# Optimization experiments

Hardware: AMD Instinct MI355X
Metric: run time of the kernel (lower is better)

Reference implementation:

```python
import jax, jax.numpy as jnp
import numpy as np

N_HEADS = 8
FACTOR = 5


def setup_inputs() -> dict:
    key = jax.random.key(0)
    ks = jax.random.split(key, 8)
    B, L, D = 2, 4096, 512
    sample_k = min(FACTOR * int(np.ceil(np.log(L))), L)  # 45
    inp = {
        "queries": jax.random.normal(ks[0], (B, L, D), jnp.float32),
        "keys": jax.random.normal(ks[1], (B, L, D), jnp.float32),
        "values": jax.random.normal(ks[2], (B, L, D), jnp.float32),
        "Wq": jax.random.normal(ks[3], (D, D), jnp.float32) * 0.02,
        "bq": jnp.zeros((D,), jnp.float32),
        "Wk": jax.random.normal(ks[4], (D, D), jnp.float32) * 0.02,
        "bk": jnp.zeros((D,), jnp.float32),
        "Wv": jax.random.normal(ks[5], (D, D), jnp.float32) * 0.02,
        "bv": jnp.zeros((D,), jnp.float32),
        "index_sample": jax.random.randint(ks[6], (L, sample_k), 0, L, jnp.int32),
    }
    return inp


def reference(queries, keys, values, Wq, bq, Wk, bk, Wv, bv, index_sample):
    b, l_q, d_model = queries.shape
    _, l_k, _ = keys.shape
    h = N_HEADS
    d = d_model // h
    # projections -> [b, h, l, d]
    q = (queries @ Wq + bq).reshape(b, l_q, h, d).transpose(0, 2, 1, 3)
    k = (keys @ Wk + bk).reshape(b, l_k, h, d).transpose(0, 2, 1, 3)
    v = (values @ Wv + bv).reshape(b, l_k, h, d).transpose(0, 2, 1, 3)
    n_top = min(FACTOR * int(np.ceil(np.log(l_q))), l_q)
    # --- prob_qk: sparse sampled QK ---
    # gather sampled keys per query position: [b, h, l_q, sample_k, d]
    k_sample = k[:, :, index_sample, :]
    q_k_sample = jnp.einsum('bhld,bhlsd->bhls', q, k_sample)
    # sparsity measure M(q, K) = max - mean
    m = q_k_sample.max(-1) - q_k_sample.sum(-1) / l_k  # [b, h, l_q]
    _, m_top = jax.lax.top_k(m, n_top)  # [b, h, n_top]
    q_reduce = jnp.take_along_axis(q, m_top[..., None], axis=2)  # [b, h, u, d]
    scores = jnp.einsum('bhud,bhkd->bhuk', q_reduce, k)  # [b, h, u, l_k]
    scale = float(1.0 / np.sqrt(d))
    scores = scores * scale
    # --- causal ProbMask on the selected query rows ---
    causal = jnp.triu(jnp.ones((l_q, l_k), bool), 1)
    mask = causal[m_top]  # [b, h, u, l_k]
    scores = jnp.where(mask, -jnp.inf, scores)
    attn = jax.nn.softmax(scores, axis=-1)
    # --- initial context: causal cumsum of V; scatter updated rows ---
    context = jnp.cumsum(v, axis=2)  # [b, h, l_q, d]
    upd = jnp.einsum('bhuk,bhkd->bhud', attn, v)
    bi = jnp.arange(b)[:, None, None]
    hi = jnp.arange(h)[None, :, None]
    context = context.at[bi, hi, m_top].set(upd)
    return context.transpose(0, 2, 1, 3).reshape(b, l_q, h * d)
```

## Files before the change

kernel.cpp:

```cpp
#include <hip/hip_runtime.h>
#include <math.h>

#define B  2
#define L  4096
#define D  512
#define H  8
#define DH 64
#define BH (B * H)
#define K3 1536
#define XPW 1024

typedef short s16x8 __attribute__((ext_vector_type(8)));
typedef float f32x4 __attribute__((ext_vector_type(4)));

#define AS1 __attribute__((address_space(1)))
#define AS3 __attribute__((address_space(3)))

__device__ __forceinline__ void lds_load16(const void* g, void* l) {
    __builtin_amdgcn_global_load_lds((const AS1 unsigned int*)g,
                                     (AS3 unsigned int*)l, 16, 0, 0);
}

__device__ __forceinline__ unsigned short f2bf(float x) {
    union { float f; unsigned u; } v; v.f = x;
    unsigned u = v.u;
    return (unsigned short)((u + 0x7fff + ((u >> 16) & 1)) >> 16);
}
__device__ __forceinline__ float bf2f(unsigned short h) {
    union { float f; unsigned u; } v; v.u = ((unsigned)h) << 16;
    return v.f;
}

__global__ __launch_bounds__(256)
void split_x(const float* __restrict__ q, const float* __restrict__ k,
             const float* __restrict__ v, unsigned short* __restrict__ Xp)
{
    const size_t g = (size_t)blockIdx.x * 256 + threadIdx.x;
    const size_t per = (size_t)8192 * 128;
    const int e = (int)(g / per);
    const size_t rem = g - (size_t)e * per;
    const int m  = (int)(rem >> 7);
    const int kq = (int)(rem & 127) << 2;

    const float* X = (e == 0) ? q : (e == 1) ? k : v;
    const float4 x = *(const float4*)(X + (size_t)m * 512 + kq);

    unsigned short h0 = f2bf(x.x), h1 = f2bf(x.y), h2 = f2bf(x.z), h3 = f2bf(x.w);

    unsigned short* dst = Xp + (size_t)e * 8192 * XPW + (size_t)m * XPW + kq;
    *(ushort4*)(dst) = make_ushort4(h0, h1, h2, h3);
    if (e != 2) {
        unsigned short l0 = f2bf(x.x - bf2f(h0)), l1 = f2bf(x.y - bf2f(h1));
        unsigned short l2 = f2bf(x.z - bf2f(h2)), l3 = f2bf(x.w - bf2f(h3));
        *(ushort4*)(dst + 512) = make_ushort4(l0, l1, l2, l3);
    }
}

__global__ __launch_bounds__(256)
void split_w(const float* __restrict__ wq, const float* __restrict__ wk,
             const float* __restrict__ wv, unsigned short* __restrict__ WpT)
{
    __shared__ float t[64][65];
    const int e  = blockIdx.z;
    const int k0 = blockIdx.x * 64;
    const int n0 = blockIdx.y * 64;
    const float* W = (e == 0) ? wq : (e == 1) ? wk : wv;
    const int tid = threadIdx.x;

    for (int idx = tid; idx < 64 * 16; idx += 256) {
        const int i = idx >> 4, j4 = (idx & 15) << 2;
        *(float4*)&t[i][j4] = *(const float4*)(W + (size_t)(k0 + i) * 512 + n0 + j4);
    }
    __syncthreads();

    const int n_loc = tid >> 2;
    const int kq    = (tid & 3) << 4;
    unsigned short h[16], l[16];
    #pragma unroll
    for (int tt = 0; tt < 16; tt++) {
        const float x = t[kq + tt][n_loc];
        h[tt] = f2bf(x);
        l[tt] = f2bf(x - bf2f(h[tt]));
    }
    unsigned short* base = WpT + (size_t)e * 512 * K3 + (size_t)(n0 + n_loc) * K3 + k0 + kq;
    #pragma unroll
    for (int g4 = 0; g4 < 4; g4++) {
        ushort4 hv = make_ushort4(h[g4*4], h[g4*4+1], h[g4*4+2], h[g4*4+3]);
        ushort4 lv = make_ushort4(l[g4*4], l[g4*4+1], l[g4*4+2], l[g4*4+3]);
        *(ushort4*)(base + g4*4)        = hv;
        *(ushort4*)(base + 512 + g4*4)  = lv;
        *(ushort4*)(base + 1024 + g4*4) = hv;
    }
}

__global__ __launch_bounds__(256)
void gemm_mfma(const unsigned short* __restrict__ Xp,
               const unsigned short* __restrict__ WpT,
               const float* __restrict__ bq, const float* __restrict__ bk,
               const float* __restrict__ bv,
               float* __restrict__ Qo, float* __restrict__ Ko,
               float* __restrict__ Vo)
{
    __shared__ __align__(16) unsigned short smA[4096];
    __shared__ __align__(16) unsigned short smB[4096];

    const int e = blockIdx.z;
    const float* bias = (e == 0) ? bq : (e == 1) ? bk : bv;
    float* C          = (e == 0) ? Qo : (e == 1) ? Ko : Vo;
    const unsigned short* Ag = Xp  + (size_t)e * 8192 * XPW;
    const unsigned short* Bg = WpT + (size_t)e * 512 * K3;
    const int kEnd = (e == 2) ? 512 : K3;

    const int tid  = threadIdx.x;
    const int lane = tid & 63;
    const int wid  = tid >> 6;
    const int wm   = wid & 1;
    const int wn   = wid >> 1;
    const int m0   = blockIdx.x * 128;
    const int n0g  = blockIdx.y * 128;

    const int r1 = tid >> 2;
    const int c8 = (((tid & 3) ^ ((r1 >> 1) & 3)) << 3);
    const unsigned short* agp = Ag + (size_t)(m0 + r1) * XPW + c8;
    const unsigned short* bgp = Bg + (size_t)(n0g + r1) * K3 + c8;
    unsigned short* lA1 = smA + (size_t)(tid & ~63) * 8;
    unsigned short* lA2 = lA1 + 2048;
    unsigned short* lB1 = smB + (size_t)(tid & ~63) * 8;
    unsigned short* lB2 = lB1 + 2048;

    const int r    = lane & 15;
    const int quad = lane >> 4;
    const int swz  = ((quad ^ ((lane >> 1) & 3)) << 4);
    const char* pA = (const char*)smA + (wm * 64 + r) * 64 + swz;
    const char* pB = (const char*)smB + (wn * 64 + r) * 64 + swz;

    f32x4 acc[4][4];
    #pragma unroll
    for (int i = 0; i < 4; i++)
        #pragma unroll
        for (int j = 0; j < 4; j++)
            acc[i][j] = (f32x4){0.f, 0.f, 0.f, 0.f};

    for (int k0 = 0; k0 < kEnd; k0 += 32) {
        const int kA = (k0 < 512) ? k0 : k0 - 512;
        lds_load16(agp + kA, lA1);
        lds_load16(agp + (size_t)64 * XPW + kA, lA2);
        lds_load16(bgp + k0, lB1);
        lds_load16(bgp + (size_t)64 * K3 + k0, lB2);
        __syncthreads();

        s16x8 af[4], bf[4];
        #pragma unroll
        for (int mt = 0; mt < 4; mt++) af[mt] = *(const s16x8*)(pA + mt * 1024);
        #pragma unroll
        for (int nt = 0; nt < 4; nt++) bf[nt] = *(const s16x8*)(pB + nt * 1024);
        #pragma unroll
        for (int mt = 0; mt < 4; mt++)
            #pragma unroll
            for (int nt = 0; nt < 4; nt++)
                acc[mt][nt] = __builtin_amdgcn_mfma_f32_16x16x32_bf16(
                    af[mt], bf[nt], acc[mt][nt], 0, 0, 0);
        __syncthreads();
    }

    #pragma unroll
    for (int nt = 0; nt < 4; nt++) {
        const int col = n0g + wn * 64 + nt * 16 + r;
        const float bb = bias[col];
        #pragma unroll
        for (int mt = 0; mt < 4; mt++) {
            const int row0 = m0 + wm * 64 + mt * 16 + quad * 4;
            #pragma unroll
            for (int i = 0; i < 4; i++)
                C[(size_t)(row0 + i) * 512 + col] = acc[mt][nt][i] + bb;
        }
    }
}

__global__ __launch_bounds__(256)
void sample_m(const float* __restrict__ Q, const float* __restrict__ K,
              const int* __restrict__ idx, float* __restrict__ m_out, int S)
{
    __shared__ float qs[4][DH];

    const int lane = threadIdx.x & 63;
    const int wib  = threadIdx.x >> 6;
    const int wid  = blockIdx.x * 4 + wib;
    const int l = wid & (L - 1);
    const int h = (wid >> 12) & (H - 1);
    const int b = wid >> 15;

    qs[wib][lane] = Q[((size_t)b * L + l) * D + h * DH + lane];
    __syncthreads();

    const int r4 = lane >> 2;
    const int c4 = lane & 3;

    float4 qf[4];
    {
        const float4* qv = (const float4*)qs[wib];
        #pragma unroll
        for (int i = 0; i < 4; i++) qf[i] = qv[c4 + 4 * i];
    }

    const float* Kb = K + (size_t)b * L * D + h * DH;
    const int* is = idx + (size_t)l * S;

    float vmax = -INFINITY, vsum = 0.f;
    const int passes = (S + 15) >> 4;
    for (int p = 0; p < passes; p++) {
        const int sp = p * 16 + r4;
        const bool ok = sp < S;
        const int j = ok ? is[sp] : 0;
        const float4* Krow = (const float4*)(Kb + (size_t)j * D);
        float dot = 0.f;
        #pragma unroll
        for (int i = 0; i < 4; i++) {
            const float4 kv = Krow[c4 + 4 * i];
            const float4 qq = qf[i];
            dot += qq.x * kv.x + qq.y * kv.y + qq.z * kv.z + qq.w * kv.w;
        }
        dot += __shfl_xor(dot, 1, 64);
        dot += __shfl_xor(dot, 2, 64);
        if (ok) {
            vmax = fmaxf(vmax, dot);
            if (c4 == 0) vsum += dot;
        }
    }
    #pragma unroll
    for (int off = 32; off; off >>= 1) {
        vmax = fmaxf(vmax, __shfl_xor(vmax, off, 64));
        vsum += __shfl_xor(vsum, off, 64);
    }
    if (lane == 0) m_out[wid] = vmax - vsum * (1.0f / (float)L);
}

__global__ __launch_bounds__(256)
void topk_kernel(const float* __restrict__ m_in, int* __restrict__ m_top,
                 float* __restrict__ sums, int NT)
{
    __shared__ unsigned hist[256];
    __shared__ unsigned sfx[257];
    __shared__ int sh_b, sh_rem;
    __shared__ int cnt_gt, cnt_eq;
    __shared__ int eqlist[128];

    const float* m = m_in + (size_t)blockIdx.x * L;
    const int tid = threadIdx.x;
    int* out = m_top + blockIdx.x * NT;

    if (tid < NT) sums[blockIdx.x * NT + tid] = 0.f;

    unsigned uv[16];
    #pragma unroll
    for (int k = 0; k < 16; k++) {
        const float f = m[tid + k * 256];
        const unsigned x = __float_as_uint(f);
        uv[k] = (x & 0x80000000u) ? ~x : (x | 0x80000000u);
    }

    unsigned prefix = 0;
    int rem = NT;

    for (int level = 0; level < 4; level++) {
        const int shift = 24 - level * 8;
        hist[tid] = 0;
        if (tid == 0) { cnt_gt = 0; cnt_eq = 0; }
        __syncthreads();
        #pragma unroll
        for (int k = 0; k < 16; k++) {
            const bool part = (level == 0) || ((uv[k] >> (shift + 8)) == prefix);
            if (part) atomicAdd(&hist[(uv[k] >> shift) & 255], 1u);
        }
        __syncthreads();
        if (tid < 64) {
            const unsigned s0 = hist[4*tid+0], s1 = hist[4*tid+1];
            const unsigned s2 = hist[4*tid+2], s3 = hist[4*tid+3];
            const unsigned loc = s0 + s1 + s2 + s3;
            unsigned suf = loc;
            #pragma unroll
            for (int off = 1; off < 64; off <<= 1) {
                const unsigned t = __shfl_down(suf, off, 64);
                if (tid + off < 64) suf += t;
            }
            const unsigned tail = suf - loc;
            sfx[4*tid+3] = tail + s3;
            sfx[4*tid+2] = tail + s3 + s2;
            sfx[4*tid+1] = tail + s3 + s2 + s1;
            sfx[4*tid+0] = suf;
            if (tid == 0) sfx[256] = 0;
        }
        __syncthreads();
        if (sfx[tid + 1] < (unsigned)rem && (unsigned)rem <= sfx[tid]) {
            sh_b   = tid;
            sh_rem = rem - (int)sfx[tid + 1];
        }
        __syncthreads();
        prefix = (prefix << 8) | (unsigned)sh_b;
        rem    = sh_rem;
        __syncthreads();
    }

    const unsigned T = prefix;
    const int n_gt = NT - rem;

    #pragma unroll
    for (int k = 0; k < 16; k++) {
        if (uv[k] > T) {
            const int pos = atomicAdd(&cnt_gt, 1);
            out[pos] = tid + k * 256;
        } else if (uv[k] == T) {
            const int pos = atomicAdd(&cnt_eq, 1);
            if (pos < 128) eqlist[pos] = tid + k * 256;
        }
    }
    __syncthreads();
    if (tid == 0) {
        int n = cnt_eq < 128 ? cnt_eq : 128;
        for (int r = 0; r < rem; r++) {
            int best = 0x7fffffff, bi = 0;
            for (int i = 0; i < n; i++)
                if (eqlist[i] < best) { best = eqlist[i]; bi = i; }
            out[n_gt + r] = best;
            eqlist[bi] = 0x7fffffff;
        }
    }
}

#define CH 64
__global__ __launch_bounds__(256)
void chunk_sums(const float* __restrict__ V, float* __restrict__ partial)
{
    const int c  = (blockIdx.x & 15) * 4 + (threadIdx.x >> 6);
    const int h  = (blockIdx.x >> 4) & (H - 1);
    const int b  = blockIdx.x >> 7;
    const int d  = threadIdx.x & 63;
    const float* base = V + (size_t)b * L * D + h * DH + d + (size_t)(c * CH) * D;

    float vals[CH];
    #pragma unroll
    for (int i = 0; i < CH; i++) vals[i] = base[(size_t)i * D];

    float s0 = 0.f, s1 = 0.f, s2 = 0.f, s3 = 0.f;
    #pragma unroll
    for (int i = 0; i < CH; i += 4) {
        s0 += vals[i]; s1 += vals[i+1]; s2 += vals[i+2]; s3 += vals[i+3];
    }
    partial[((size_t)((b * H + h) * 64 + c)) * DH + d] = (s0 + s1) + (s2 + s3);
}

__global__ __launch_bounds__(256)
void cumsum_write(const float* __restrict__ V, const float* __restrict__ partial,
                  float* __restrict__ out)
{
    const int c  = (blockIdx.x & 15) * 4 + (threadIdx.x >> 6);
    const int h  = (blockIdx.x >> 4) & (H - 1);
    const int b  = blockIdx.x >> 7;
    const int d  = threadIdx.x & 63;
    const size_t off = (size_t)b * L * D + h * DH + d + (size_t)(c * CH) * D;
    const float* base  = V   + off;
    float*       obase = out + off;
    const float* pb = partial + (size_t)((b * H + h) * 64) * DH + d;

    float vals[CH];
    #pragma unroll
    for (int i = 0; i < CH; i++) vals[i] = base[(size_t)i * D];

    float acc = 0.f;
    for (int cc = 0; cc < c; cc++) acc += pb[cc * DH];

    #pragma unroll
    for (int i = 0; i < CH; i++) {
        acc += vals[i];
        obase[(size_t)i * D] = acc;
    }
}

__global__ __launch_bounds__(256)
void attn_scores(const float* __restrict__ Q, const float* __restrict__ K,
                 const int* __restrict__ m_top, float* __restrict__ scores,
                 float* __restrict__ sums, float* __restrict__ out, int NT)
{
    __shared__ float qsh[15][DH];
    __shared__ int   psh[15];

    const int bh = blockIdx.z;
    const int h  = bh & (H - 1);
    const int b  = bh >> 3;
    const int ug = blockIdx.y;
    const int j0 = blockIdx.x * 512;
    const int tid = threadIdx.x;

    for (int i = tid; i < 15 * DH; i += 256) {
        const int u = i >> 6, d = i & 63;
        const int p = m_top[bh * NT + ug * 15 + u];
        if (d == 0) psh[u] = p;
        qsh[u][d] = Q[((size_t)b * L + p) * D + h * DH + d];
    }
    __syncthreads();

    if (blockIdx.x == 0) {
        for (int i = tid; i < 15 * DH; i += 256) {
            const int u = i >> 6, d = i & 63;
            out[((size_t)b * L + psh[u]) * D + h * DH + d] = 0.f;
        }
    }

    const float* Kb = K + (size_t)b * L * D + h * DH;
    const int ja = j0 + tid;
    const int jb = ja + 256;
    float4 k0[16], k1[16];
    {
        const float4* ra = (const float4*)(Kb + (size_t)ja * D);
        const float4* rb = (const float4*)(Kb + (size_t)jb * D);
        #pragma unroll
        for (int i = 0; i < 16; i++) { k0[i] = ra[i]; k1[i] = rb[i]; }
    }

    for (int u = 0; u < 15; u++) {
        const int p = psh[u];
        const float4* qv = (const float4*)qsh[u];
        float d0 = 0.f, d1 = 0.f;
        #pragma unroll
        for (int i = 0; i < 16; i++) {
            const float4 q4 = qv[i];
            d0 += q4.x * k0[i].x + q4.y * k0[i].y + q4.z * k0[i].z + q4.w * k0[i].w;
            d1 += q4.x * k1[i].x + q4.y * k1[i].y + q4.z * k1[i].z + q4.w * k1[i].w;
        }
        const float e0 = (ja <= p) ? __expf(d0 * 0.125f) : 0.f;
        const float e1 = (jb <= p) ? __expf(d1 * 0.125f) : 0.f;
        float* srow = scores + (size_t)(bh * NT + ug * 15 + u) * L;
        srow[ja] = e0;
        srow[jb] = e1;
        float t = e0 + e1;
        #pragma unroll
        for (int off = 32; off; off >>= 1) t += __shfl_xor(t, off, 64);
        if ((tid & 63) == 0) atomicAdd(&sums[bh * NT + ug * 15 + u], t);
    }
}

__global__ __launch_bounds__(256)
void attn_wv(const float* __restrict__ scores, const float* __restrict__ V,
             const int* __restrict__ m_top, const float* __restrict__ sums,
             float* __restrict__ out, int NT)
{
    __shared__ float ssh[45][64];
    __shared__ float sinv[45];
    __shared__ int   psh[45];

    const int bh = blockIdx.y;
    const int h  = bh & (H - 1);
    const int b  = bh >> 3;
    const int j0 = blockIdx.x * 64;
    const int tid = threadIdx.x;
    const int d   = tid & 63;
    const int w   = tid >> 6;

    if (tid < NT) {
        psh[tid]  = m_top[bh * NT + tid];
        sinv[tid] = 1.0f / sums[bh * NT + tid];
    }

    const float* Vb = V + (size_t)b * L * D + h * DH + d;
    float vreg[64];
    #pragma unroll
    for (int i = 0; i < 64; i++) vreg[i] = Vb[(size_t)(j0 + i) * D];

    __syncthreads();
    for (int i = tid; i < NT * 64; i += 256) {
        const int u = i >> 6, j = i & 63;
        ssh[u][j] = scores[(size_t)(bh * NT + u) * L + j0 + j] * sinv[u];
    }
    __syncthreads();

    for (int u = w; u < NT; u += 4) {
        const int p = psh[u];
        if (p < j0) continue;
        const float* wt = ssh[u];
        float acc = 0.f;
        #pragma unroll
        for (int i = 0; i < 64; i++) acc += wt[i] * vreg[i];
        atomicAdd(out + ((size_t)b * L + p) * D + h * DH + d, acc);
    }
}

extern "C" void kernel_launch(void* const* d_in, const int* in_sizes, int n_in,
                              void* d_out, int out_size, void* d_ws, size_t ws_size,
                              hipStream_t stream)
{
    const float* queries = (const float*)d_in[0];
    const float* keys    = (const float*)d_in[1];
    const float* values  = (const float*)d_in[2];
    const float* Wq      = (const float*)d_in[3];
    const float* bq      = (const float*)d_in[4];
    const float* Wk      = (const float*)d_in[5];
    const float* bk      = (const float*)d_in[6];
    const float* Wv      = (const float*)d_in[7];
    const float* bv      = (const float*)d_in[8];
    const int*   idx     = (const int*)d_in[9];
    float* out = (float*)d_out;

    const int S  = in_sizes[9] / L;
    const int NT = S;

    const size_t NE = (size_t)B * L * D;
    float* Qb      = (float*)d_ws;
    float* Kb      = Qb + NE;
    float* Vb      = Kb + NE;
    float* m_buf   = Vb + NE;
    float* cs_part = m_buf + (size_t)BH * L;
    int*   m_top   = (int*)(cs_part + (size_t)BH * 64 * DH);
    float* scores  = (float*)(m_top + 1024);
    float* sums    = scores + (size_t)BH * NT * L;
    unsigned short* Xp  = (unsigned short*)(sums + 1024);
    unsigned short* WpT = Xp + (size_t)3 * 8192 * XPW;

    split_x<<<3 * 8192 * 128 / 256, 256, 0, stream>>>(queries, keys, values, Xp);
    split_w<<<dim3(8, 8, 3), 256, 0, stream>>>(Wq, Wk, Wv, WpT);

    gemm_mfma<<<dim3(8192 / 128, 512 / 128, 3), 256, 0, stream>>>(
        Xp, WpT, bq, bk, bv, Qb, Kb, Vb);

    sample_m<<<BH * L / 4, 256, 0, stream>>>(Qb, Kb, idx, m_buf, S);

    topk_kernel<<<BH, 256, 0, stream>>>(m_buf, m_top, sums, NT);

    chunk_sums<<<BH * 16, 256, 0, stream>>>(Vb, cs_part);
    cumsum_write<<<BH * 16, 256, 0, stream>>>(Vb, cs_part, out);

    attn_scores<<<dim3(8, 3, BH), 256, 0, stream>>>(Qb, Kb, m_top, scores, sums, out, NT);
    attn_wv<<<dim3(64, BH), 256, 0, stream>>>(scores, Vb, m_top, sums, out, NT);
}
```

Baseline: 277.2 us.

## Fuse attention score and weighted-V kernels, dropping the intermediate scores buffer

Merges attn_scores and attn_wv into one attn_fused kernel. Each block holds 256 keys and 256 value rows in registers and, for every selected query, computes exp scores, reduces the softmax denominators atomically, and accumulates the weighted V directly into the output. This removes the round trip of the full scores matrix through global memory and one kernel launch. Zeroing of the selected output rows moves into cumsum_write via a per-position flag array written by topk, and a small attn_norm kernel divides by the sums afterwards. The cost is more atomics on output rows and a serial loop over all 45 queries per block.

```diff
diff --git a/kernel.cpp b/kernel.cpp
--- a/kernel.cpp
+++ b/kernel.cpp
@@ -237,7 +237,7 @@
 
 __global__ __launch_bounds__(256)
 void topk_kernel(const float* __restrict__ m_in, int* __restrict__ m_top,
-                 float* __restrict__ sums, int NT)
+                 float* __restrict__ sums, int* __restrict__ flags, int NT)
 {
     __shared__ unsigned hist[256];
     __shared__ unsigned sfx[257];
@@ -248,8 +248,10 @@
     const float* m = m_in + (size_t)blockIdx.x * L;
     const int tid = threadIdx.x;
     int* out = m_top + blockIdx.x * NT;
+    int* fl  = flags + (size_t)blockIdx.x * L;
 
     if (tid < NT) sums[blockIdx.x * NT + tid] = 0.f;
+    for (int i = tid; i < L; i += 256) fl[i] = 0;
 
     unsigned uv[16];
     #pragma unroll
@@ -325,6 +327,8 @@
             eqlist[bi] = 0x7fffffff;
         }
     }
+    __syncthreads();
+    if (tid < NT) fl[out[tid]] = 1;
 }
 
 #define CH 64
@@ -351,7 +355,7 @@
 
 __global__ __launch_bounds__(256)
 void cumsum_write(const float* __restrict__ V, const float* __restrict__ partial,
-                  float* __restrict__ out)
+                  const int* __restrict__ flags, float* __restrict__ out)
 {
     const int c  = (blockIdx.x & 15) * 4 + (threadIdx.x >> 6);
     const int h  = (blockIdx.x >> 4) & (H - 1);
@@ -361,6 +365,7 @@
     const float* base  = V   + off;
     float*       obase = out + off;
     const float* pb = partial + (size_t)((b * H + h) * 64) * DH + d;
+    const int*   fp = flags + (size_t)(b * H + h) * L + c * CH;
 
     float vals[CH];
     #pragma unroll
@@ -372,116 +377,88 @@
     #pragma unroll
     for (int i = 0; i < CH; i++) {
         acc += vals[i];
-        obase[(size_t)i * D] = acc;
-    }
-}
-
-__global__ __launch_bounds__(256)
-void attn_scores(const float* __restrict__ Q, const float* __restrict__ K,
-                 const int* __restrict__ m_top, float* __restrict__ scores,
-                 float* __restrict__ sums, float* __restrict__ out, int NT)
-{
-    __shared__ float qsh[15][DH];
-    __shared__ int   psh[15];
-
-    const int bh = blockIdx.z;
-    const int h  = bh & (H - 1);
-    const int b  = bh >> 3;
-    const int ug = blockIdx.y;
-    const int j0 = blockIdx.x * 512;
-    const int tid = threadIdx.x;
-
-    for (int i = tid; i < 15 * DH; i += 256) {
-        const int u = i >> 6, d = i & 63;
-        const int p = m_top[bh * NT + ug * 15 + u];
-        if (d == 0) psh[u] = p;
-        qsh[u][d] = Q[((size_t)b * L + p) * D + h * DH + d];
-    }
-    __syncthreads();
-
-    if (blockIdx.x == 0) {
-        for (int i = tid; i < 15 * DH; i += 256) {
-            const int u = i >> 6, d = i & 63;
-            out[((size_t)b * L + psh[u]) * D + h * DH + d] = 0.f;
-        }
-    }
-
-    const float* Kb = K + (size_t)b * L * D + h * DH;
-    const int ja = j0 + tid;
-    const int jb = ja + 256;
-    float4 k0[16], k1[16];
-    {
-        const float4* ra = (const float4*)(Kb + (size_t)ja * D);
-        const float4* rb = (const float4*)(Kb + (size_t)jb * D);
-        #pragma unroll
-        for (int i = 0; i < 16; i++) { k0[i] = ra[i]; k1[i] = rb[i]; }
-    }
-
-    for (int u = 0; u < 15; u++) {
-        const int p = psh[u];
-        const float4* qv = (const float4*)qsh[u];
-        float d0 = 0.f, d1 = 0.f;
-        #pragma unroll
-        for (int i = 0; i < 16; i++) {
-            const float4 q4 = qv[i];
-            d0 += q4.x * k0[i].x + q4.y * k0[i].y + q4.z * k0[i].z + q4.w * k0[i].w;
-            d1 += q4.x * k1[i].x + q4.y * k1[i].y + q4.z * k1[i].z + q4.w * k1[i].w;
-        }
-        const float e0 = (ja <= p) ? __expf(d0 * 0.125f) : 0.f;
-        const float e1 = (jb <= p) ? __expf(d1 * 0.125f) : 0.f;
-        float* srow = scores + (size_t)(bh * NT + ug * 15 + u) * L;
-        srow[ja] = e0;
-        srow[jb] = e1;
-        float t = e0 + e1;
-        #pragma unroll
-        for (int off = 32; off; off >>= 1) t += __shfl_xor(t, off, 64);
-        if ((tid & 63) == 0) atomicAdd(&sums[bh * NT + ug * 15 + u], t);
-    }
-}
-
-__global__ __launch_bounds__(256)
-void attn_wv(const float* __restrict__ scores, const float* __restrict__ V,
-             const int* __restrict__ m_top, const float* __restrict__ sums,
-             float* __restrict__ out, int NT)
-{
-    __shared__ float ssh[45][64];
-    __shared__ float sinv[45];
+        obase[(size_t)i * D] = fp[i] ? 0.f : acc;
+    }
+}
+
+__global__ __launch_bounds__(256)
+void attn_fused(const float* __restrict__ Q, const float* __restrict__ K,
+                const float* __restrict__ V, const int* __restrict__ m_top,
+                float* __restrict__ sums, float* __restrict__ out, int NT)
+{
+    __shared__ float qsh[45][DH];
     __shared__ int   psh[45];
+    __shared__ float ssh[256];
 
     const int bh = blockIdx.y;
     const int h  = bh & (H - 1);
     const int b  = bh >> 3;
-    const int j0 = blockIdx.x * 64;
+    const int j0 = blockIdx.x * 256;
     const int tid = threadIdx.x;
     const int d   = tid & 63;
     const int w   = tid >> 6;
 
-    if (tid < NT) {
-        psh[tid]  = m_top[bh * NT + tid];
-        sinv[tid] = 1.0f / sums[bh * NT + tid];
-    }
-
+    for (int i = tid; i < NT * DH; i += 256) {
+        const int u = i >> 6, dd = i & 63;
+        const int p = m_top[bh * NT + u];
+        if (dd == 0) psh[u] = p;
+        qsh[u][dd] = Q[((size_t)b * L + p) * D + h * DH + dd];
+    }
+
+    const float* Kb = K + (size_t)b * L * D + h * DH;
+    float4 kreg[16];
+    {
+        const float4* kr = (const float4*)(Kb + (size_t)(j0 + tid) * D);
+        #pragma unroll
+        for (int i = 0; i < 16; i++) kreg[i] = kr[i];
+    }
     const float* Vb = V + (size_t)b * L * D + h * DH + d;
+    const int jb = j0 + w * 64;
     float vreg[64];
     #pragma unroll
-    for (int i = 0; i < 64; i++) vreg[i] = Vb[(size_t)(j0 + i) * D];
-
+    for (int i = 0; i < 64; i++) vreg[i] = Vb[(size_t)(jb + i) * D];
     __syncthreads();
-    for (int i = tid; i < NT * 64; i += 256) {
-        const int u = i >> 6, j = i & 63;
-        ssh[u][j] = scores[(size_t)(bh * NT + u) * L + j0 + j] * sinv[u];
-    }
-    __syncthreads();
-
-    for (int u = w; u < NT; u += 4) {
+
+    const int j = j0 + tid;
+    float* obase = out + (size_t)b * L * D + h * DH;
+
+    for (int u = 0; u < NT; u++) {
         const int p = psh[u];
-        if (p < j0) continue;
-        const float* wt = ssh[u];
+        if (p < jb) continue;
+        const float4* qv = (const float4*)qsh[u];
+        float dot = 0.f;
+        #pragma unroll
+        for (int i = 0; i < 16; i++) {
+            const float4 q4 = qv[i];
+            dot += q4.x * kreg[i].x + q4.y * kreg[i].y
+                 + q4.z * kreg[i].z + q4.w * kreg[i].w;
+        }
+        const float e = (j <= p) ? __expf(dot * 0.125f) : 0.f;
+        ssh[tid] = e;
+        float t = e;
+        #pragma unroll
+        for (int off = 32; off; off >>= 1) t += __shfl_xor(t, off, 64);
+        if (d == 0) atomicAdd(&sums[bh * NT + u], t);
+
+        const float* wts = &ssh[w * 64];
         float acc = 0.f;
         #pragma unroll
-        for (int i = 0; i < 64; i++) acc += wt[i] * vreg[i];
-        atomicAdd(out + ((size_t)b * L + p) * D + h * DH + d, acc);
-    }
+        for (int i = 0; i < 64; i++) acc += wts[i] * vreg[i];
+        atomicAdd(obase + (size_t)p * D + d, acc);
+    }
+}
+
+__global__ __launch_bounds__(64)
+void attn_norm(const int* __restrict__ m_top, const float* __restrict__ sums,
+               float* __restrict__ out, int NT)
+{
+    const int gu = blockIdx.x;
+    const int bh = gu / NT;
+    const int h  = bh & (H - 1);
+    const int b  = bh >> 3;
+    const int p  = m_top[gu];
+    float* row = out + ((size_t)b * L + p) * D + h * DH;
+    row[threadIdx.x] /= sums[gu];
 }
 
 extern "C" void kernel_launch(void* const* d_in, const int* in_sizes, int n_in,
@@ -510,9 +487,9 @@
     float* m_buf   = Vb + NE;
     float* cs_part = m_buf + (size_t)BH * L;
     int*   m_top   = (int*)(cs_part + (size_t)BH * 64 * DH);
-    float* scores  = (float*)(m_top + 1024);
-    float* sums    = scores + (size_t)BH * NT * L;
-    unsigned short* Xp  = (unsigned short*)(sums + 1024);
+    float* sums    = (float*)(m_top + 1024);
+    int*   flags   = (int*)(sums + 1024);
+    unsigned short* Xp  = (unsigned short*)(flags + (size_t)BH * L);
     unsigned short* WpT = Xp + (size_t)3 * 8192 * XPW;
 
     split_x<<<3 * 8192 * 128 / 256, 256, 0, stream>>>(queries, keys, values, Xp);
@@ -523,11 +500,11 @@
 
     sample_m<<<BH * L / 4, 256, 0, stream>>>(Qb, Kb, idx, m_buf, S);
 
-    topk_kernel<<<BH, 256, 0, stream>>>(m_buf, m_top, sums, NT);
+    topk_kernel<<<BH, 256, 0, stream>>>(m_buf, m_top, sums, flags, NT);
 
     chunk_sums<<<BH * 16, 256, 0, stream>>>(Vb, cs_part);
-    cumsum_write<<<BH * 16, 256, 0, stream>>>(Vb, cs_part, out);
-
-    attn_scores<<<dim3(8, 3, BH), 256, 0, stream>>>(Qb, Kb, m_top, scores, sums, out, NT);
-    attn_wv<<<dim3(64, BH), 256, 0, stream>>>(scores, Vb, m_top, sums, out, NT);
-}
+    cumsum_write<<<BH * 16, 256, 0, stream>>>(Vb, cs_part, flags, out);
+
+    attn_fused<<<dim3(16, BH), 256, 0, stream>>>(Qb, Kb, Vb, m_top, sums, out, NT);
+    attn_norm<<<BH * NT, 64, 0, stream>>>(m_top, sums, out, NT);
+}
```

Result: slower. 290.8 us (+4.9%).

## Merge independent kernels into combined launches and replace row zeroing with flags

Applied to the files above, without the earlier changes.

Merges split_x and split_w into one launch, chunk_sums and sample_m into one, and cumsum_write and attn_scores into one. The merged kernels branch on block index, so independent work shares a launch and can overlap. To remove the ordering dependency between zeroing the selected rows and writing the cumsum, topk now writes a per-position flag array and cumsum writes zero where the flag is set. This cuts kernel launches and inter-kernel gaps, at the cost of extra flag memory traffic and more register and shared-memory pressure in the merged kernels.

```diff
diff --git a/kernel.cpp b/kernel.cpp
--- a/kernel.cpp
+++ b/kernel.cpp
@@ -32,64 +32,64 @@
 }
 
 __global__ __launch_bounds__(256)
-void split_x(const float* __restrict__ q, const float* __restrict__ k,
-             const float* __restrict__ v, unsigned short* __restrict__ Xp)
-{
-    const size_t g = (size_t)blockIdx.x * 256 + threadIdx.x;
-    const size_t per = (size_t)8192 * 128;
-    const int e = (int)(g / per);
-    const size_t rem = g - (size_t)e * per;
-    const int m  = (int)(rem >> 7);
-    const int kq = (int)(rem & 127) << 2;
-
-    const float* X = (e == 0) ? q : (e == 1) ? k : v;
-    const float4 x = *(const float4*)(X + (size_t)m * 512 + kq);
-
-    unsigned short h0 = f2bf(x.x), h1 = f2bf(x.y), h2 = f2bf(x.z), h3 = f2bf(x.w);
-
-    unsigned short* dst = Xp + (size_t)e * 8192 * XPW + (size_t)m * XPW + kq;
-    *(ushort4*)(dst) = make_ushort4(h0, h1, h2, h3);
-    if (e != 2) {
-        unsigned short l0 = f2bf(x.x - bf2f(h0)), l1 = f2bf(x.y - bf2f(h1));
-        unsigned short l2 = f2bf(x.z - bf2f(h2)), l3 = f2bf(x.w - bf2f(h3));
-        *(ushort4*)(dst + 512) = make_ushort4(l0, l1, l2, l3);
-    }
-}
-
-__global__ __launch_bounds__(256)
-void split_w(const float* __restrict__ wq, const float* __restrict__ wk,
-             const float* __restrict__ wv, unsigned short* __restrict__ WpT)
-{
-    __shared__ float t[64][65];
-    const int e  = blockIdx.z;
-    const int k0 = blockIdx.x * 64;
-    const int n0 = blockIdx.y * 64;
-    const float* W = (e == 0) ? wq : (e == 1) ? wk : wv;
+void k_split(const float* __restrict__ q, const float* __restrict__ k,
+             const float* __restrict__ v,
+             const float* __restrict__ wq, const float* __restrict__ wk,
+             const float* __restrict__ wv,
+             unsigned short* __restrict__ Xp, unsigned short* __restrict__ WpT)
+{
     const int tid = threadIdx.x;
-
-    for (int idx = tid; idx < 64 * 16; idx += 256) {
-        const int i = idx >> 4, j4 = (idx & 15) << 2;
-        *(float4*)&t[i][j4] = *(const float4*)(W + (size_t)(k0 + i) * 512 + n0 + j4);
-    }
-    __syncthreads();
-
-    const int n_loc = tid >> 2;
-    const int kq    = (tid & 3) << 4;
-    unsigned short h[16], l[16];
-    #pragma unroll
-    for (int tt = 0; tt < 16; tt++) {
-        const float x = t[kq + tt][n_loc];
-        h[tt] = f2bf(x);
-        l[tt] = f2bf(x - bf2f(h[tt]));
-    }
-    unsigned short* base = WpT + (size_t)e * 512 * K3 + (size_t)(n0 + n_loc) * K3 + k0 + kq;
-    #pragma unroll
-    for (int g4 = 0; g4 < 4; g4++) {
-        ushort4 hv = make_ushort4(h[g4*4], h[g4*4+1], h[g4*4+2], h[g4*4+3]);
-        ushort4 lv = make_ushort4(l[g4*4], l[g4*4+1], l[g4*4+2], l[g4*4+3]);
-        *(ushort4*)(base + g4*4)        = hv;
-        *(ushort4*)(base + 512 + g4*4)  = lv;
-        *(ushort4*)(base + 1024 + g4*4) = hv;
+    if (blockIdx.x < 192) {
+        __shared__ float t[64][65];
+        const int bx = blockIdx.x;
+        const int e  = bx >> 6;
+        const int k0 = (bx & 7) * 64;
+        const int n0 = ((bx >> 3) & 7) * 64;
+        const float* W = (e == 0) ? wq : (e == 1) ? wk : wv;
+
+        for (int idx = tid; idx < 64 * 16; idx += 256) {
+            const int i = idx >> 4, j4 = (idx & 15) << 2;
+            *(float4*)&t[i][j4] = *(const float4*)(W + (size_t)(k0 + i) * 512 + n0 + j4);
+        }
+        __syncthreads();
+
+        const int n_loc = tid >> 2;
+        const int kq    = (tid & 3) << 4;
+        unsigned short h[16], l[16];
+        #pragma unroll
+        for (int tt = 0; tt < 16; tt++) {
+            const float x = t[kq + tt][n_loc];
+            h[tt] = f2bf(x);
+            l[tt] = f2bf(x - bf2f(h[tt]));
+        }
+        unsigned short* base = WpT + (size_t)e * 512 * K3 + (size_t)(n0 + n_loc) * K3 + k0 + kq;
+        #pragma unroll
+        for (int g4 = 0; g4 < 4; g4++) {
+            ushort4 hv = make_ushort4(h[g4*4], h[g4*4+1], h[g4*4+2], h[g4*4+3]);
+            ushort4 lv = make_ushort4(l[g4*4], l[g4*4+1], l[g4*4+2], l[g4*4+3]);
+            *(ushort4*)(base + g4*4)        = hv;
+            *(ushort4*)(base + 512 + g4*4)  = lv;
+            *(ushort4*)(base + 1024 + g4*4) = hv;
+        }
+    } else {
+        const size_t g = (size_t)(blockIdx.x - 192) * 256 + tid;
+        const size_t per = (size_t)8192 * 128;
+        const int e = (int)(g / per);
+        const size_t rem = g - (size_t)e * per;
+        const int m  = (int)(rem >> 7);
+        const int kq = (int)(rem & 127) << 2;
+
+        const float* X = (e == 0) ? q : (e == 1) ? k : v;
+        const float4 x = *(const float4*)(X + (size_t)m * 512 + kq);
+
+        unsigned short h0 = f2bf(x.x), h1 = f2bf(x.y), h2 = f2bf(x.z), h3 = f2bf(x.w);
+        unsigned short* dst = Xp + (size_t)e * 8192 * XPW + (size_t)m * XPW + kq;
+        *(ushort4*)(dst) = make_ushort4(h0, h1, h2, h3);
+        if (e != 2) {
+            unsigned short l0 = f2bf(x.x - bf2f(h0)), l1 = f2bf(x.y - bf2f(h1));
+            unsigned short l2 = f2bf(x.z - bf2f(h2)), l3 = f2bf(x.w - bf2f(h3));
+            *(ushort4*)(dst + 512) = make_ushort4(l0, l1, l2, l3);
+        }
     }
 }
 
@@ -177,67 +177,89 @@
     }
 }
 
+#define CH 64
 __global__ __launch_bounds__(256)
-void sample_m(const float* __restrict__ Q, const float* __restrict__ K,
-              const int* __restrict__ idx, float* __restrict__ m_out, int S)
-{
-    __shared__ float qs[4][DH];
-
-    const int lane = threadIdx.x & 63;
-    const int wib  = threadIdx.x >> 6;
-    const int wid  = blockIdx.x * 4 + wib;
-    const int l = wid & (L - 1);
-    const int h = (wid >> 12) & (H - 1);
-    const int b = wid >> 15;
-
-    qs[wib][lane] = Q[((size_t)b * L + l) * D + h * DH + lane];
-    __syncthreads();
-
-    const int r4 = lane >> 2;
-    const int c4 = lane & 3;
-
-    float4 qf[4];
-    {
-        const float4* qv = (const float4*)qs[wib];
-        #pragma unroll
-        for (int i = 0; i < 4; i++) qf[i] = qv[c4 + 4 * i];
-    }
-
-    const float* Kb = K + (size_t)b * L * D + h * DH;
-    const int* is = idx + (size_t)l * S;
-
-    float vmax = -INFINITY, vsum = 0.f;
-    const int passes = (S + 15) >> 4;
-    for (int p = 0; p < passes; p++) {
-        const int sp = p * 16 + r4;
-        const bool ok = sp < S;
-        const int j = ok ? is[sp] : 0;
-        const float4* Krow = (const float4*)(Kb + (size_t)j * D);
-        float dot = 0.f;
-        #pragma unroll
-        for (int i = 0; i < 4; i++) {
-            const float4 kv = Krow[c4 + 4 * i];
-            const float4 qq = qf[i];
-            dot += qq.x * kv.x + qq.y * kv.y + qq.z * kv.z + qq.w * kv.w;
-        }
-        dot += __shfl_xor(dot, 1, 64);
-        dot += __shfl_xor(dot, 2, 64);
-        if (ok) {
-            vmax = fmaxf(vmax, dot);
-            if (c4 == 0) vsum += dot;
-        }
-    }
-    #pragma unroll
-    for (int off = 32; off; off >>= 1) {
-        vmax = fmaxf(vmax, __shfl_xor(vmax, off, 64));
-        vsum += __shfl_xor(vsum, off, 64);
-    }
-    if (lane == 0) m_out[wid] = vmax - vsum * (1.0f / (float)L);
+void k_sample_chunks(const float* __restrict__ Q, const float* __restrict__ K,
+                     const int* __restrict__ idx, float* __restrict__ m_out, int S,
+                     const float* __restrict__ V, float* __restrict__ partial)
+{
+    const int tid = threadIdx.x;
+    if (blockIdx.x < 256) {
+        const int bid = blockIdx.x;
+        const int c  = (bid & 15) * 4 + (tid >> 6);
+        const int h  = (bid >> 4) & (H - 1);
+        const int b  = bid >> 7;
+        const int d  = tid & 63;
+        const float* base = V + (size_t)b * L * D + h * DH + d + (size_t)(c * CH) * D;
+
+        float vals[CH];
+        #pragma unroll
+        for (int i = 0; i < CH; i++) vals[i] = base[(size_t)i * D];
+
+        float s0 = 0.f, s1 = 0.f, s2 = 0.f, s3 = 0.f;
+        #pragma unroll
+        for (int i = 0; i < CH; i += 4) {
+            s0 += vals[i]; s1 += vals[i+1]; s2 += vals[i+2]; s3 += vals[i+3];
+        }
+        partial[((size_t)((b * H + h) * 64 + c)) * DH + d] = (s0 + s1) + (s2 + s3);
+    } else {
+        __shared__ float qs[4][DH];
+        const int lane = tid & 63;
+        const int wib  = tid >> 6;
+        const int wid  = (blockIdx.x - 256) * 4 + wib;
+        const int l = wid & (L - 1);
+        const int h = (wid >> 12) & (H - 1);
+        const int b = wid >> 15;
+
+        qs[wib][lane] = Q[((size_t)b * L + l) * D + h * DH + lane];
+        __syncthreads();
+
+        const int r4 = lane >> 2;
+        const int c4 = lane & 3;
+
+        float4 qf[4];
+        {
+            const float4* qv = (const float4*)qs[wib];
+            #pragma unroll
+            for (int i = 0; i < 4; i++) qf[i] = qv[c4 + 4 * i];
+        }
+
+        const float* Kb = K + (size_t)b * L * D + h * DH;
+        const int* is = idx + (size_t)l * S;
+
+        float vmax = -INFINITY, vsum = 0.f;
+        const int passes = (S + 15) >> 4;
+        for (int p = 0; p < passes; p++) {
+            const int sp = p * 16 + r4;
+            const bool ok = sp < S;
+            const int j = ok ? is[sp] : 0;
+            const float4* Krow = (const float4*)(Kb + (size_t)j * D);
+            float dot = 0.f;
+            #pragma unroll
+            for (int i = 0; i < 4; i++) {
+                const float4 kv = Krow[c4 + 4 * i];
+                const float4 qq = qf[i];
+                dot += qq.x * kv.x + qq.y * kv.y + qq.z * kv.z + qq.w * kv.w;
+            }
+            dot += __shfl_xor(dot, 1, 64);
+            dot += __shfl_xor(dot, 2, 64);
+            if (ok) {
+                vmax = fmaxf(vmax, dot);
+                if (c4 == 0) vsum += dot;
+            }
+        }
+        #pragma unroll
+        for (int off = 32; off; off >>= 1) {
+            vmax = fmaxf(vmax, __shfl_xor(vmax, off, 64));
+            vsum += __shfl_xor(vsum, off, 64);
+        }
+        if (lane == 0) m_out[wid] = vmax - vsum * (1.0f / (float)L);
+    }
 }
 
 __global__ __launch_bounds__(256)
 void topk_kernel(const float* __restrict__ m_in, int* __restrict__ m_top,
-                 float* __restrict__ sums, int NT)
+                 float* __restrict__ sums, int* __restrict__ flags, int NT)
 {
     __shared__ unsigned hist[256];
     __shared__ unsigned sfx[257];
@@ -248,8 +270,10 @@
     const float* m = m_in + (size_t)blockIdx.x * L;
     const int tid = threadIdx.x;
     int* out = m_top + blockIdx.x * NT;
+    int* fl  = flags + (size_t)blockIdx.x * L;
 
     if (tid < NT) sums[blockIdx.x * NT + tid] = 0.f;
+    for (int i = tid; i < L; i += 256) fl[i] = 0;
 
     unsigned uv[16];
     #pragma unroll
@@ -325,117 +349,94 @@
             eqlist[bi] = 0x7fffffff;
         }
     }
-}
-
-#define CH 64
+    __syncthreads();
+    if (tid < NT) fl[out[tid]] = 1;
+}
+
 __global__ __launch_bounds__(256)
-void chunk_sums(const float* __restrict__ V, float* __restrict__ partial)
-{
-    const int c  = (blockIdx.x & 15) * 4 + (threadIdx.x >> 6);
-    const int h  = (blockIdx.x >> 4) & (H - 1);
-    const int b  = blockIdx.x >> 7;
-    const int d  = threadIdx.x & 63;
-    const float* base = V + (size_t)b * L * D + h * DH + d + (size_t)(c * CH) * D;
-
-    float vals[CH];
-    #pragma unroll
-    for (int i = 0; i < CH; i++) vals[i] = base[(size_t)i * D];
-
-    float s0 = 0.f, s1 = 0.f, s2 = 0.f, s3 = 0.f;
-    #pragma unroll
-    for (int i = 0; i < CH; i += 4) {
-        s0 += vals[i]; s1 += vals[i+1]; s2 += vals[i+2]; s3 += vals[i+3];
-    }
-    partial[((size_t)((b * H + h) * 64 + c)) * DH + d] = (s0 + s1) + (s2 + s3);
-}
-
-__global__ __launch_bounds__(256)
-void cumsum_write(const float* __restrict__ V, const float* __restrict__ partial,
-                  float* __restrict__ out)
-{
-    const int c  = (blockIdx.x & 15) * 4 + (threadIdx.x >> 6);
-    const int h  = (blockIdx.x >> 4) & (H - 1);
-    const int b  = blockIdx.x >> 7;
-    const int d  = threadIdx.x & 63;
-    const size_t off = (size_t)b * L * D + h * DH + d + (size_t)(c * CH) * D;
-    const float* base  = V   + off;
-    float*       obase = out + off;
-    const float* pb = partial + (size_t)((b * H + h) * 64) * DH + d;
-
-    float vals[CH];
-    #pragma unroll
-    for (int i = 0; i < CH; i++) vals[i] = base[(size_t)i * D];
-
-    float acc = 0.f;
-    for (int cc = 0; cc < c; cc++) acc += pb[cc * DH];
-
-    #pragma unroll
-    for (int i = 0; i < CH; i++) {
-        acc += vals[i];
-        obase[(size_t)i * D] = acc;
-    }
-}
-
-__global__ __launch_bounds__(256)
-void attn_scores(const float* __restrict__ Q, const float* __restrict__ K,
-                 const int* __restrict__ m_top, float* __restrict__ scores,
-                 float* __restrict__ sums, float* __restrict__ out, int NT)
-{
-    __shared__ float qsh[15][DH];
-    __shared__ int   psh[15];
-
-    const int bh = blockIdx.z;
-    const int h  = bh & (H - 1);
-    const int b  = bh >> 3;
-    const int ug = blockIdx.y;
-    const int j0 = blockIdx.x * 512;
+void k_cumsum_scores(const float* __restrict__ V, const float* __restrict__ partial,
+                     const int* __restrict__ flags, float* __restrict__ out,
+                     const float* __restrict__ Q, const float* __restrict__ K,
+                     const int* __restrict__ m_top, float* __restrict__ scores,
+                     float* __restrict__ sums, int NT)
+{
     const int tid = threadIdx.x;
-
-    for (int i = tid; i < 15 * DH; i += 256) {
-        const int u = i >> 6, d = i & 63;
-        const int p = m_top[bh * NT + ug * 15 + u];
-        if (d == 0) psh[u] = p;
-        qsh[u][d] = Q[((size_t)b * L + p) * D + h * DH + d];
-    }
-    __syncthreads();
-
-    if (blockIdx.x == 0) {
+    if (blockIdx.x < 256) {
+        const int bid = blockIdx.x;
+        const int c  = (bid & 15) * 4 + (tid >> 6);
+        const int h  = (bid >> 4) & (H - 1);
+        const int b  = bid >> 7;
+        const int d  = tid & 63;
+        const size_t off = (size_t)b * L * D + h * DH + d + (size_t)(c * CH) * D;
+        const float* base  = V   + off;
+        float*       obase = out + off;
+        const float* pb = partial + (size_t)((b * H + h) * 64) * DH + d;
+        const int*   fp = flags + (size_t)(b * H + h) * L + c * CH;
+
+        float vals[CH];
+        #pragma unroll
+        for (int i = 0; i < CH; i++) vals[i] = base[(size_t)i * D];
+
+        float acc = 0.f;
+        for (int cc = 0; cc < c; cc++) acc += pb[cc * DH];
+
+        #pragma unroll
+        for (int i = 0; i < CH; i++) {
+            acc += vals[i];
+            obase[(size_t)i * D] = fp[i] ? 0.f : acc;
+        }
+    } else {
+        __shared__ float qsh[15][DH];
+        __shared__ int   psh[15];
+
+        const int rem2 = blockIdx.x - 256;
+        const int bh = rem2 / 24;
+        const int r2 = rem2 % 24;
+        const int ug = r2 >> 3;
+        const int jc = r2 & 7;
+        const int h  = bh & (H - 1);
+        const int b  = bh >> 3;
+        const int j0 = jc * 512;
+
         for (int i = tid; i < 15 * DH; i += 256) {
             const int u = i >> 6, d = i & 63;
-            out[((size_t)b * L + psh[u]) * D + h * DH + d] = 0.f;
-        }
-    }
-
-    const float* Kb = K + (size_t)b * L * D + h * DH;
-    const int ja = j0 + tid;
-    const int jb = ja + 256;
-    float4 k0[16], k1[16];
-    {
-        const float4* ra = (const float4*)(Kb + (size_t)ja * D);
-        const float4* rb = (const float4*)(Kb + (size_t)jb * D);
-        #pragma unroll
-        for (int i = 0; i < 16; i++) { k0[i] = ra[i]; k1[i] = rb[i]; }
-    }
-
-    for (int u = 0; u < 15; u++) {
-        const int p = psh[u];
-        const float4* qv = (const float4*)qsh[u];
-        float d0 = 0.f, d1 = 0.f;
-        #pragma unroll
-        for (int i = 0; i < 16; i++) {
-            const float4 q4 = qv[i];
-            d0 += q4.x * k0[i].x + q4.y * k0[i].y + q4.z * k0[i].z + q4.w * k0[i].w;
-            d1 += q4.x * k1[i].x + q4.y * k1[i].y + q4.z * k1[i].z + q4.w * k1[i].w;
-        }
-        const float e0 = (ja <= p) ? __expf(d0 * 0.125f) : 0.f;
-        const float e1 = (jb <= p) ? __expf(d1 * 0.125f) : 0.f;
-        float* srow = scores + (size_t)(bh * NT + ug * 15 + u) * L;
-        srow[ja] = e0;
-        srow[jb] = e1;
-        float t = e0 + e1;
-        #pragma unroll
-        for (int off = 32; off; off >>= 1) t += __shfl_xor(t, off, 64);
-        if ((tid & 63) == 0) atomicAdd(&sums[bh * NT + ug * 15 + u], t);
+            const int p = m_top[bh * NT + ug * 15 + u];
+            if (d == 0) psh[u] = p;
+            qsh[u][d] = Q[((size_t)b * L + p) * D + h * DH + d];
+        }
+        __syncthreads();
+
+        const float* Kb = K + (size_t)b * L * D + h * DH;
+        const int ja = j0 + tid;
+        const int jb = ja + 256;
+        float4 k0[16], k1[16];
+        {
+            const float4* ra = (const float4*)(Kb + (size_t)ja * D);
+            const float4* rb = (const float4*)(Kb + (size_t)jb * D);
+            #pragma unroll
+            for (int i = 0; i < 16; i++) { k0[i] = ra[i]; k1[i] = rb[i]; }
+        }
+
+        for (int u = 0; u < 15; u++) {
+            const int p = psh[u];
+            const float4* qv = (const float4*)qsh[u];
+            float d0 = 0.f, d1 = 0.f;
+            #pragma unroll
+            for (int i = 0; i < 16; i++) {
+                const float4 q4 = qv[i];
+                d0 += q4.x * k0[i].x + q4.y * k0[i].y + q4.z * k0[i].z + q4.w * k0[i].w;
+                d1 += q4.x * k1[i].x + q4.y * k1[i].y + q4.z * k1[i].z + q4.w * k1[i].w;
+            }
+            const float e0 = (ja <= p) ? __expf(d0 * 0.125f) : 0.f;
+            const float e1 = (jb <= p) ? __expf(d1 * 0.125f) : 0.f;
+            float* srow = scores + (size_t)(bh * NT + ug * 15 + u) * L;
+            srow[ja] = e0;
+            srow[jb] = e1;
+            float t = e0 + e1;
+            #pragma unroll
+            for (int off = 32; off; off >>= 1) t += __shfl_xor(t, off, 64);
+            if ((tid & 63) == 0) atomicAdd(&sums[bh * NT + ug * 15 + u], t);
+        }
     }
 }
 
@@ -510,24 +511,25 @@
     float* m_buf   = Vb + NE;
     float* cs_part = m_buf + (size_t)BH * L;
     int*   m_top   = (int*)(cs_part + (size_t)BH * 64 * DH);
-    float* scores  = (float*)(m_top + 1024);
-    float* sums    = scores + (size_t)BH * NT * L;
-    unsigned short* Xp  = (unsigned short*)(sums + 1024);
+    float* sums    = (float*)(m_top + 1024);
+    int*   flags   = (int*)(sums + 1024);
+    float* scores  = (float*)(flags + (size_t)BH * L);
+    unsigned short* Xp  = (unsigned short*)(scores + (size_t)BH * NT * L);
     unsigned short* WpT = Xp + (size_t)3 * 8192 * XPW;
 
-    split_x<<<3 * 8192 * 128 / 256, 256, 0, stream>>>(queries, keys, values, Xp);
-    split_w<<<dim3(8, 8, 3), 256, 0, stream>>>(Wq, Wk, Wv, WpT);
+    k_split<<<192 + 3 * 8192 * 128 / 256, 256, 0, stream>>>(
+        queries, keys, values, Wq, Wk, Wv, Xp, WpT);
 
     gemm_mfma<<<dim3(8192 / 128, 512 / 128, 3), 256, 0, stream>>>(
         Xp, WpT, bq, bk, bv, Qb, Kb, Vb);
 
-    sample_m<<<BH * L / 4, 256, 0, stream>>>(Qb, Kb, idx, m_buf, S);
-
-    topk_kernel<<<BH, 256, 0, stream>>>(m_buf, m_top, sums, NT);
-
-    chunk_sums<<<BH * 16, 256, 0, stream>>>(Vb, cs_part);
-    cumsum_write<<<BH * 16, 256, 0, stream>>>(Vb, cs_part, out);
-
-    attn_scores<<<dim3(8, 3, BH), 256, 0, stream>>>(Qb, Kb, m_top, scores, sums, out, NT);
+    k_sample_chunks<<<256 + BH * L / 4, 256, 0, stream>>>(
+        Qb, Kb, idx, m_buf, S, Vb, cs_part);
+
+    topk_kernel<<<BH, 256, 0, stream>>>(m_buf, m_top, sums, flags, NT);
+
+    k_cumsum_scores<<<256 + 384, 256, 0, stream>>>(
+        Vb, cs_part, flags, out, Qb, Kb, m_top, scores, sums, NT);
+
     attn_wv<<<dim3(64, BH), 256, 0, stream>>>(scores, Vb, m_top, sums, out, NT);
 }
```

Measured after the change: 273.5 us. Within noise of the previous version (-1.3%).
